# Performance work log

Measured on AMD Instinct MI355X. Metric: run time of the kernel, lower is better.

The kernel has to match this reference:

```python
import jax, jax.numpy as jnp
import numpy as np

B, T, V, E, H, D = 2048, 50, 65, 100, 20, 5  # batch, block, vocab, n_embd, heads, head_size


def setup_inputs() -> dict:
    key = jax.random.key(0)
    ks = jax.random.split(key, 12)
    idx = jax.random.randint(ks[0], (B, T), 0, V)
    targets = jax.random.randint(ks[1], (B, T), 0, V)
    tok_emb = jax.random.normal(ks[2], (V, E), dtype=jnp.float32) * 0.02
    pos_emb = jax.random.normal(ks[3], (T, E), dtype=jnp.float32) * 0.02
    # per-head Linear(N_EMBD, head_size, bias=False) weights, stacked over heads: [H, D, E]
    Wk = jax.random.normal(ks[4], (H, D, E), dtype=jnp.float32) * 0.1
    Wq = jax.random.normal(ks[5], (H, D, E), dtype=jnp.float32) * 0.1
    Wv = jax.random.normal(ks[6], (H, D, E), dtype=jnp.float32) * 0.1
    W_ff = jax.random.normal(ks[7], (E, E), dtype=jnp.float32) * 0.1
    b_ff = jnp.zeros((E,), dtype=jnp.float32)
    W_lm = jax.random.normal(ks[8], (V, E), dtype=jnp.float32) * 0.1
    b_lm = jnp.zeros((V,), dtype=jnp.float32)
    return {"idx": idx, "targets": targets, "tok_emb": tok_emb, "pos_emb": pos_emb,
            "Wk": Wk, "Wq": Wq, "Wv": Wv, "W_ff": W_ff, "b_ff": b_ff,
            "W_lm": W_lm, "b_lm": b_lm}


def reference(idx, targets, tok_emb, pos_emb, Wk, Wq, Wv, W_ff, b_ff, W_lm, b_lm):
    Bs, Ts = idx.shape
    x = tok_emb[idx] + pos_emb[:Ts]  # [B, T, E]
    # batched over all heads (equivalent to the per-head Python loop + concat)
    k = jnp.einsum('bte,hde->bhtd', x, Wk)
    q = jnp.einsum('bte,hde->bhtd', x, Wq)
    v = jnp.einsum('bte,hde->bhtd', x, Wv)
    # NOTE: faithful to original: k @ q^T, scaled by C**0.5 (multiply, C = N_EMBD)
    scale = jnp.asarray(E, x.dtype) ** 0.5
    w = jnp.einsum('bhtd,bhsd->bhts', k, q) * scale  # [B, H, T, S]
    tril = jnp.tril(jnp.ones((Ts, Ts), dtype=bool))
    w = jnp.where(tril, w, -jnp.inf)
    # original: torch.softmax(weights, dim=1) on [B, T, S] -> axis 't' here (axis=2)
    w = jax.nn.softmax(w, axis=2)
    attn = jnp.einsum('bhts,bhsd->bhtd', w, v)
    attn = attn.transpose(0, 2, 1, 3).reshape(Bs, Ts, H * D)  # concat heads -> [B, T, E]
    h = jax.nn.relu(attn @ W_ff.T + b_ff)  # FeedForward applied AFTER attention
    logits = h @ W_lm.T + b_lm  # [B, T, V]
    logits2d = logits.reshape(Bs * Ts, V)
    tflat = targets.reshape(Bs * Ts)
    logp = jax.nn.log_softmax(logits2d, axis=-1)
    loss = -jnp.take_along_axis(logp, tflat[:, None], axis=-1).mean()
    return (logits2d, loss)
```

## Files before the change

kernel.cpp:

```cpp
#include <hip/hip_runtime.h>
#include <hip/hip_bf16.h>

#define Bb 2048
#define Tt 50
#define Vv 65
#define Ee 100
#define Hh 20
#define Dd 5

typedef __bf16 v8bf __attribute__((ext_vector_type(8)));
typedef short v8s __attribute__((ext_vector_type(8)));
typedef short v4s __attribute__((ext_vector_type(4)));
typedef float f32x4 __attribute__((ext_vector_type(4)));

__device__ __forceinline__ v8bf bzero8() {
    v8s z = {0, 0, 0, 0, 0, 0, 0, 0};
    union { v8s s; v8bf b; } u; u.s = z; return u.b;
}
__device__ __forceinline__ unsigned short bfbits(float f) {
    union { __hip_bfloat16 h; unsigned short s; } c;
    c.h = __float2bfloat16(f);
    return c.s;
}
__device__ __forceinline__ float bf2f(short s) {
    union { unsigned i; float f; } c; c.i = ((unsigned)(unsigned short)s) << 16; return c.f;
}
__device__ __forceinline__ unsigned pack2(float a, float b) {
    return (unsigned)bfbits(a) | ((unsigned)bfbits(b) << 16);
}

__device__ __forceinline__ f32x4 mfma_16x16x16_bf16(v4s a, v4s b, f32x4 c) {
#if __has_builtin(__builtin_amdgcn_mfma_f32_16x16x16bf16_1k)
    return __builtin_amdgcn_mfma_f32_16x16x16bf16_1k(a, b, c, 0, 0, 0);
#else
    f32x4 d;
    asm volatile("v_mfma_f32_16x16x16_bf16 %0, %1, %2, %3\n\ts_nop 7\n\ts_nop 4"
                 : "=v"(d) : "v"(a), "v"(b), "v"(c));
    return d;
#endif
}

#define WS_WKQV 1024
#define WS_WFF  (1024 + 81920)
#define WS_WLM  (1024 + 81920 + 32768)

#define XSTR 136
#define R2 8000
#define R3 16000
#define VSTR 52

__global__ __launch_bounds__(256) void prep_kernel(
    const float* __restrict__ Wk, const float* __restrict__ Wq,
    const float* __restrict__ Wv, const float* __restrict__ Wff,
    const float* __restrict__ Wlm, char* __restrict__ ws,
    float* __restrict__ out)
{
    int g = blockIdx.x * 256 + threadIdx.x;
    if (g == 0) out[Bb * Tt * Vv] = 0.f;
    __hip_bfloat16* wkqv = (__hip_bfloat16*)(ws + WS_WKQV);
    __hip_bfloat16* wff  = (__hip_bfloat16*)(ws + WS_WFF);
    __hip_bfloat16* wlm  = (__hip_bfloat16*)(ws + WS_WLM);
    if (g < 40960) {
        int n = g >> 7, e = g & 127;
        float v = 0.f;
        if (e < Ee) {
            if (n < 100)      v = Wk[n * Ee + e] * 14.4269504089f;
            else if (n < 200) v = Wq[(n - 100) * Ee + e];
            else if (n < 300) v = Wv[(n - 200) * Ee + e];
        }
        wkqv[g] = __float2bfloat16(v);
    } else if (g < 57344) {
        int gg = g - 40960; int n = gg >> 7, e = gg & 127;
        float v = (e < Ee && n < Ee) ? Wff[n * Ee + e] : 0.f;
        wff[gg] = __float2bfloat16(v);
    } else {
        int gg = g - 57344; int n = gg >> 7, e = gg & 127;
        float v = (e < Ee && n < Vv) ? Wlm[n * Ee + e] : 0.f;
        wlm[gg] = __float2bfloat16(v);
    }
}

__global__ __launch_bounds__(256, 3) void gpt_main(
    const int* __restrict__ idx, const int* __restrict__ targets,
    const float* __restrict__ tok_emb, const float* __restrict__ pos_emb,
    const float* __restrict__ b_ff, const float* __restrict__ b_lm,
    const char* __restrict__ ws, float* __restrict__ out)
{
    __shared__ __attribute__((aligned(16))) __hip_bfloat16 sh[21200];
    __shared__ int tok_s[Tt];
    __shared__ float bsum;

    const int b    = blockIdx.x;
    const int tid  = threadIdx.x;
    const int wave = tid >> 6;
    const int ln   = tid & 15;
    const int quad = (tid >> 4) & 3;

    if (tid < Tt) tok_s[tid] = idx[b * Tt + tid];
    if (tid == 0) bsum = 0.f;
    __syncthreads();
    for (int i = tid; i < Tt * 32; i += 256) {
        int r = i >> 5, c4 = (i & 31) * 4;
        ushort4 o;
        if (c4 < Ee) {
            const float4 te = *(const float4*)&tok_emb[tok_s[r] * Ee + c4];
            const float4 pe = *(const float4*)&pos_emb[r * Ee + c4];
            o.x = bfbits(te.x + pe.x); o.y = bfbits(te.y + pe.y);
            o.z = bfbits(te.z + pe.z); o.w = bfbits(te.w + pe.w);
        } else {
            o.x = 0; o.y = 0; o.z = 0; o.w = 0;
        }
        *(ushort4*)&sh[r * XSTR + c4] = o;
    }
    __syncthreads();

    {
        const __hip_bfloat16* wkqv = (const __hip_bfloat16*)(ws + WS_WKQV);
        f32x4 acc[5][4];
#pragma unroll
        for (int j = 0; j < 5; ++j)
#pragma unroll
            for (int mt = 0; mt < 4; ++mt) {
                f32x4 z = {0.f, 0.f, 0.f, 0.f};
                acc[j][mt] = z;
            }
#pragma unroll
        for (int kt = 0; kt < 4; ++kt) {
            v8bf a[4];
#pragma unroll
            for (int mt = 0; mt < 4; ++mt)
                a[mt] = (mt < 3 || ln < 2)
                      ? *(const v8bf*)&sh[(mt * 16 + ln) * XSTR + kt * 32 + quad * 8]
                      : bzero8();
#pragma unroll
            for (int j = 0; j < 5; ++j) {
                int nt = wave * 5 + j;
                v8bf bfr = *(const v8bf*)&wkqv[(nt * 16 + ln) * 128 + kt * 32 + quad * 8];
#pragma unroll
                for (int mt = 0; mt < 4; ++mt)
                    acc[j][mt] = __builtin_amdgcn_mfma_f32_16x16x32_bf16(a[mt], bfr, acc[j][mt], 0, 0, 0);
            }
        }
        __syncthreads();
        for (int i = tid; i < 2000; i += 256) {
            int off = (i < 1000) ? i * 8 : R2 + (i - 1000) * 8;
            *(unsigned short*)&sh[off + 5] = 0;
            *(unsigned*)&sh[off + 6] = 0;
        }
#pragma unroll
        for (int j = 0; j < 5; ++j) {
            int n = (wave * 5 + j) * 16 + ln;
            if (n < 300) {
                int mat = n / 100;
                int jj  = n - mat * 100;
                int h   = jj / 5, d = jj - (jj / 5) * 5;
                if (mat == 2) {
                    int base = R3 + (h * 5 + d) * VSTR;
#pragma unroll
                    for (int mt = 0; mt < 4; ++mt) {
                        if (mt < 3 || quad == 0) {
                            float v0 = acc[j][mt][0], v1 = acc[j][mt][1];
                            float v2 = acc[j][mt][2], v3 = acc[j][mt][3];
                            if (mt == 3) { v2 = 0.f; v3 = 0.f; }
                            uint2 pk = make_uint2(pack2(v0, v1), pack2(v2, v3));
                            *(uint2*)&sh[base + mt * 16 + quad * 4] = pk;
                        }
                    }
                } else {
                    int roff = (mat == 0) ? R2 : 0;
                    int rbase = h * 50;
#pragma unroll
                    for (int mt = 0; mt < 4; ++mt)
#pragma unroll
                        for (int r = 0; r < 4; ++r) {
                            int m = mt * 16 + quad * 4 + r;
                            if (m < Tt)
                                sh[roff + (rbase + m) * 8 + d] = __float2bfloat16(acc[j][mt][r]);
                        }
                }
            }
        }
    }
    __syncthreads();

    unsigned attp[5][8];
    {
        const float BIGF = 3.0e38f;
        float dA1[4], d50[4];
#pragma unroll
        for (int r = 0; r < 4; ++r) {
            int qr = quad * 4 + r;
            dA1[r] = (ln >= qr) ? BIGF : 0.f;
            d50[r] = (qr < 2)  ? BIGF : 0.f;
        }
        const float tl3 = (ln < 2) ? BIGF : 0.f;

#pragma unroll
        for (int hj = 0; hj < 5; ++hj) {
            const int h = wave * 5 + hj;
            v8bf qf[4], kf[4];
#pragma unroll
            for (int i = 0; i < 4; ++i) {
                int row = i * 16 + ln;
                qf[i] = (quad == 0) ? *(const v8bf*)&sh[(h * 50 + row) * 8] : bzero8();
                kf[i] = (quad == 0) ? *(const v8bf*)&sh[R2 + (h * 50 + row) * 8] : bzero8();
            }
            f32x4 pac[4];
#pragma unroll
            for (int mt = 0; mt < 4; ++mt) { f32x4 z = {0.f, 0.f, 0.f, 0.f}; pac[mt] = z; }
#pragma unroll
            for (int ms = 0; ms < 4; ++ms) {
                float esum[4] = {0.f, 0.f, 0.f, 0.f};
                v4s afs[4];
#pragma unroll
                for (int u = 0; u < 4 - ms; ++u) {
                    f32x4 z = {0.f, 0.f, 0.f, 0.f};
                    f32x4 t1 = __builtin_amdgcn_mfma_f32_16x16x32_bf16(qf[ms], kf[ms + u], z, 0, 0, 0);
                    v4s af;
#pragma unroll
                    for (int r = 0; r < 4; ++r) {
                        float x = __builtin_amdgcn_exp2f(t1[r]);
                        if (u == 0)      x = fminf(x, dA1[r]);
                        if (ms + u == 3) x = fminf(x, tl3);
                        if (ms == 3)     x = fminf(x, d50[r]);
                        esum[r] += x;
                        af[r] = (short)bfbits(x);
                    }
                    afs[u] = af;
                }
#pragma unroll
                for (int r = 0; r < 4; ++r) {
                    float e = esum[r];
                    e += __shfl_xor(e, 1);
                    e += __shfl_xor(e, 2);
                    e += __shfl_xor(e, 4);
                    e += __shfl_xor(e, 8);
                    esum[r] = e;
                }
                float rdv[4];
#pragma unroll
                for (int r = 0; r < 4; ++r)
                    rdv[r] = (ms < 3 || (quad * 4 + r) < 2)
                           ? __builtin_amdgcn_rcpf(esum[r]) : 0.f;
                v4s braw;
                if (ln < Dd && (ms < 3 || quad == 0))
                    braw = *(const v4s*)&sh[R3 + (h * 5 + ln) * VSTR + ms * 16 + quad * 4];
                else { v4s zz = {0, 0, 0, 0}; braw = zz; }
                v4s bvt;
#pragma unroll
                for (int j = 0; j < 4; ++j)
                    bvt[j] = (short)bfbits(bf2f(braw[j]) * rdv[j]);
#pragma unroll
                for (int u = 0; u < 4 - ms; ++u)
                    pac[ms + u] = mfma_16x16x16_bf16(afs[u], bvt, pac[ms + u]);
            }
#pragma unroll
            for (int mt = 0; mt < 4; ++mt) {
                attp[hj][mt * 2]     = pack2(pac[mt][0], pac[mt][1]);
                attp[hj][mt * 2 + 1] = pack2(pac[mt][2], pac[mt][3]);
            }
        }
    }
    __syncthreads();

#pragma unroll
    for (int hj = 0; hj < 5; ++hj) {
        int col = (wave * 5 + hj) * 5 + ln;
#pragma unroll
        for (int mt = 0; mt < 4; ++mt)
#pragma unroll
            for (int r = 0; r < 4; ++r) {
                int t = mt * 16 + quad * 4 + r;
                if (ln < Dd && t < Tt) {
                    unsigned w = attp[hj][mt * 2 + (r >> 1)];
                    unsigned short v = (unsigned short)((r & 1) ? (w >> 16) : (w & 0xffff));
                    *(unsigned short*)&sh[t * XSTR + col] = v;
                }
            }
    }
    __syncthreads();

    {
        const __hip_bfloat16* wff = (const __hip_bfloat16*)(ws + WS_WFF);
        f32x4 fac[2][4];
#pragma unroll
        for (int u = 0; u < 2; ++u)
#pragma unroll
            for (int mt = 0; mt < 4; ++mt) {
                f32x4 z = {0.f, 0.f, 0.f, 0.f};
                fac[u][mt] = z;
            }
        const int nn = (wave < 3) ? 2 : 1;
#pragma unroll
        for (int kt = 0; kt < 4; ++kt) {
            v8bf a[4];
#pragma unroll
            for (int mt = 0; mt < 4; ++mt)
                a[mt] = (mt < 3 || ln < 2)
                      ? *(const v8bf*)&sh[(mt * 16 + ln) * XSTR + kt * 32 + quad * 8]
                      : bzero8();
#pragma unroll
            for (int u = 0; u < 2; ++u) {
                if (u < nn) {
                    int nt = wave + u * 4;
                    v8bf bfr = *(const v8bf*)&wff[(nt * 16 + ln) * 128 + kt * 32 + quad * 8];
#pragma unroll
                    for (int mt = 0; mt < 4; ++mt)
                        fac[u][mt] = __builtin_amdgcn_mfma_f32_16x16x32_bf16(a[mt], bfr, fac[u][mt], 0, 0, 0);
                }
            }
        }
#pragma unroll
        for (int u = 0; u < 2; ++u) {
            if (u < nn) {
                int n = (wave + u * 4) * 16 + ln;
                if (n < Ee) {
                    float bias = b_ff[n];
#pragma unroll
                    for (int mt = 0; mt < 4; ++mt)
#pragma unroll
                        for (int r = 0; r < 4; ++r) {
                            int m = mt * 16 + quad * 4 + r;
                            if (m < Tt) {
                                float v = fac[u][mt][r] + bias;
                                sh[R2 + m * XSTR + n] = __float2bfloat16(v > 0.f ? v : 0.f);
                            }
                        }
                }
            }
        }
    }
    __syncthreads();

    {
        const __hip_bfloat16* wlm = (const __hip_bfloat16*)(ws + WS_WLM);
        float* lgl = (float*)sh;
#pragma unroll
        for (int i = 0; i < 5; ++i) {
            int job = wave + i * 4;
            int mt = job / 5, nt = job - (job / 5) * 5;
            f32x4 acc = {0.f, 0.f, 0.f, 0.f};
#pragma unroll
            for (int kt = 0; kt < 4; ++kt) {
                v8bf a = (mt < 3 || ln < 2)
                       ? *(const v8bf*)&sh[R2 + (mt * 16 + ln) * XSTR + kt * 32 + quad * 8]
                       : bzero8();
                v8bf bf = *(const v8bf*)&wlm[(nt * 16 + ln) * 128 + kt * 32 + quad * 8];
                acc = __builtin_amdgcn_mfma_f32_16x16x32_bf16(a, bf, acc, 0, 0, 0);
            }
            int n = nt * 16 + ln;
            if (n < Vv) {
                float bias = b_lm[n];
#pragma unroll
                for (int r = 0; r < 4; ++r) {
                    int m = mt * 16 + quad * 4 + r;
                    if (m < Tt) {
                        float v = acc[r] + bias;
                        out[(b * Tt + m) * Vv + n] = v;
                        lgl[m * 68 + n] = v;
                    }
                }
            }
        }
    }
    __syncthreads();

    if (tid < 200) {
        int r = tid >> 2, lv = tid & 3;
        const float* row = (const float*)sh + r * 68;
        float mx = -3.0e38f;
        for (int v = lv; v < Vv; v += 4) mx = fmaxf(mx, row[v]);
        mx = fmaxf(mx, __shfl_xor(mx, 1));
        mx = fmaxf(mx, __shfl_xor(mx, 2));
        float sum = 0.f;
        for (int v = lv; v < Vv; v += 4)
            sum += __builtin_amdgcn_exp2f((row[v] - mx) * 1.4426950408889634f);
        sum += __shfl_xor(sum, 1);
        sum += __shfl_xor(sum, 2);
        if (lv == 0) {
            float lse = mx + 0.69314718055994531f * log2f(sum);
            int tgt = targets[b * Tt + r];
            atomicAdd(&bsum, lse - row[tgt]);
        }
    }
    __syncthreads();
    if (tid == 0)
        atomicAdd(&out[Bb * Tt * Vv], bsum * (1.0f / (float)(Bb * Tt)));
}

extern "C" void kernel_launch(void* const* d_in, const int* in_sizes, int n_in,
                              void* d_out, int out_size, void* d_ws, size_t ws_size,
                              hipStream_t stream)
{
    const int* idx     = (const int*)d_in[0];
    const int* targets = (const int*)d_in[1];
    const float* tok_emb = (const float*)d_in[2];
    const float* pos_emb = (const float*)d_in[3];
    const float* Wk  = (const float*)d_in[4];
    const float* Wq  = (const float*)d_in[5];
    const float* Wv  = (const float*)d_in[6];
    const float* Wff = (const float*)d_in[7];
    const float* bff = (const float*)d_in[8];
    const float* Wlm = (const float*)d_in[9];
    const float* blm = (const float*)d_in[10];
    float* out = (float*)d_out;
    char* ws = (char*)d_ws;

    hipLaunchKernelGGL(prep_kernel, dim3(264), dim3(256), 0, stream, Wk, Wq, Wv, Wff, Wlm, ws, out);
    hipLaunchKernelGGL(gpt_main, dim3(Bb), dim3(256), 0, stream,
                       idx, targets, tok_emb, pos_emb, bff, blm, (const char*)ws, out);
}
```

Before: 181.5 us.

## Compact Q/K shared layout to shrink LDS and raise occupancy to four blocks

```diff
diff --git a/kernel.cpp b/kernel.cpp
--- a/kernel.cpp
+++ b/kernel.cpp
@@ -45,8 +45,12 @@
 #define WS_WLM  (1024 + 81920 + 32768)
 
 #define XSTR 136
-#define R2 8000
-#define R3 16000
+#define QLO 0
+#define QHI 4000
+#define KLO 5000
+#define KHI 9000
+#define R3V 10000
+#define HST 6800
 #define VSTR 52
 
 __global__ __launch_bounds__(256) void prep_kernel(
@@ -80,13 +84,13 @@
     }
 }
 
-__global__ __launch_bounds__(256, 3) void gpt_main(
+__global__ __launch_bounds__(256, 4) void gpt_main(
     const int* __restrict__ idx, const int* __restrict__ targets,
     const float* __restrict__ tok_emb, const float* __restrict__ pos_emb,
     const float* __restrict__ b_ff, const float* __restrict__ b_lm,
     const char* __restrict__ ws, float* __restrict__ out)
 {
-    __shared__ __attribute__((aligned(16))) __hip_bfloat16 sh[21200];
+    __shared__ __attribute__((aligned(16))) __hip_bfloat16 sh[15200];
     __shared__ int tok_s[Tt];
     __shared__ float bsum;
 
@@ -142,11 +146,6 @@
             }
         }
         __syncthreads();
-        for (int i = tid; i < 2000; i += 256) {
-            int off = (i < 1000) ? i * 8 : R2 + (i - 1000) * 8;
-            *(unsigned short*)&sh[off + 5] = 0;
-            *(unsigned*)&sh[off + 6] = 0;
-        }
 #pragma unroll
         for (int j = 0; j < 5; ++j) {
             int n = (wave * 5 + j) * 16 + ln;
@@ -155,7 +154,7 @@
                 int jj  = n - mat * 100;
                 int h   = jj / 5, d = jj - (jj / 5) * 5;
                 if (mat == 2) {
-                    int base = R3 + (h * 5 + d) * VSTR;
+                    int base = R3V + (h * 5 + d) * VSTR;
 #pragma unroll
                     for (int mt = 0; mt < 4; ++mt) {
                         if (mt < 3 || quad == 0) {
@@ -167,15 +166,19 @@
                         }
                     }
                 } else {
-                    int roff = (mat == 0) ? R2 : 0;
+                    int lo = (mat == 0) ? KLO : QLO;
+                    int hi = (mat == 0) ? KHI : QHI;
                     int rbase = h * 50;
 #pragma unroll
                     for (int mt = 0; mt < 4; ++mt)
 #pragma unroll
                         for (int r = 0; r < 4; ++r) {
                             int m = mt * 16 + quad * 4 + r;
-                            if (m < Tt)
-                                sh[roff + (rbase + m) * 8 + d] = __float2bfloat16(acc[j][mt][r]);
+                            if (m < Tt) {
+                                __hip_bfloat16 val = __float2bfloat16(acc[j][mt][r]);
+                                if (d < 4) sh[lo + (rbase + m) * 4 + d] = val;
+                                else       sh[hi + rbase + m] = val;
+                            }
                         }
                 }
             }
@@ -201,9 +204,17 @@
             v8bf qf[4], kf[4];
 #pragma unroll
             for (int i = 0; i < 4; ++i) {
-                int row = i * 16 + ln;
-                qf[i] = (quad == 0) ? *(const v8bf*)&sh[(h * 50 + row) * 8] : bzero8();
-                kf[i] = (quad == 0) ? *(const v8bf*)&sh[R2 + (h * 50 + row) * 8] : bzero8();
+                int row = h * 50 + i * 16 + ln;
+                if (quad == 0) {
+                    union { unsigned long long u[2]; v8bf b; } uq, uk;
+                    uq.u[0] = *(const unsigned long long*)&sh[QLO + row * 4];
+                    uq.u[1] = (unsigned long long)*(const unsigned short*)&sh[QHI + row];
+                    uk.u[0] = *(const unsigned long long*)&sh[KLO + row * 4];
+                    uk.u[1] = (unsigned long long)*(const unsigned short*)&sh[KHI + row];
+                    qf[i] = uq.b; kf[i] = uk.b;
+                } else {
+                    qf[i] = bzero8(); kf[i] = bzero8();
+                }
             }
             f32x4 pac[4];
 #pragma unroll
@@ -244,7 +255,7 @@
                            ? __builtin_amdgcn_rcpf(esum[r]) : 0.f;
                 v4s braw;
                 if (ln < Dd && (ms < 3 || quad == 0))
-                    braw = *(const v4s*)&sh[R3 + (h * 5 + ln) * VSTR + ms * 16 + quad * 4];
+                    braw = *(const v4s*)&sh[R3V + (h * 5 + ln) * VSTR + ms * 16 + quad * 4];
                 else { v4s zz = {0, 0, 0, 0}; braw = zz; }
                 v4s bvt;
 #pragma unroll
@@ -323,7 +334,7 @@
                             int m = mt * 16 + quad * 4 + r;
                             if (m < Tt) {
                                 float v = fac[u][mt][r] + bias;
-                                sh[R2 + m * XSTR + n] = __float2bfloat16(v > 0.f ? v : 0.f);
+                                sh[HST + m * XSTR + n] = __float2bfloat16(v > 0.f ? v : 0.f);
                             }
                         }
                 }
@@ -343,7 +354,7 @@
 #pragma unroll
             for (int kt = 0; kt < 4; ++kt) {
                 v8bf a = (mt < 3 || ln < 2)
-                       ? *(const v8bf*)&sh[R2 + (mt * 16 + ln) * XSTR + kt * 32 + quad * 8]
+                       ? *(const v8bf*)&sh[HST + (mt * 16 + ln) * XSTR + kt * 32 + quad * 8]
                        : bzero8();
                 v8bf bf = *(const v8bf*)&wlm[(nt * 16 + ln) * 128 + kt * 32 + quad * 8];
                 acc = __builtin_amdgcn_mfma_f32_16x16x32_bf16(a, bf, acc, 0, 0, 0);
```

Measured after the change: 193.3 us. 1.07x slower.
